# Optimization experiments

Hardware: AMD Instinct MI355X
Metric: run time of the kernel (lower is better)

The kernel has to match this reference:

```python
import jax, jax.numpy as jnp
import numpy as np

N_PDE = 4096
SENSOR_RANGE = 0.08
WINDOW = int(SENSOR_RANGE * N_PDE)   # 327
HALF = WINDOW // 2                   # 163
RESIZE_LEN = 20
FREQS = jnp.array([1.0, 2.0, 4.0, 8.0], dtype=jnp.float32)
EPS = 1e-6  # flax GroupNorm default epsilon
U_MAX, V_MAX = 40.0, 1.0
N_AGENTS = 262144


def setup_inputs() -> dict:
    key = jax.random.key(0)
    ks = jax.random.split(key, 16)

    def w(k, shape):
        fan_in = shape[0]
        return (jax.random.normal(k, shape, jnp.float32) / np.float32(np.sqrt(fan_in)))

    return {
        "z_curr": jax.random.normal(ks[0], (N_PDE,), jnp.float32),
        "z_target": jax.random.normal(ks[1], (N_PDE,), jnp.float32),
        "xi_curr": jax.random.uniform(ks[2], (N_AGENTS,), jnp.float32),
        # branch net (features=[256,256]), each layer: Dense + GroupNorm(1 group) + tanh
        "bW0": w(ks[3], (2 * RESIZE_LEN, 256)), "bb0": jnp.zeros((256,), jnp.float32),
        "bs0": jnp.ones((256,), jnp.float32), "bB0": jnp.zeros((256,), jnp.float32),
        "bW1": w(ks[4], (256, 256)), "bb1": jnp.zeros((256,), jnp.float32),
        "bs1": jnp.ones((256,), jnp.float32), "bB1": jnp.zeros((256,), jnp.float32),
        # trunk net: 8 -> 32 -> 32
        "tW0": w(ks[5], (8, 32)), "tb0": jnp.zeros((32,), jnp.float32),
        "tW1": w(ks[6], (32, 32)), "tb1": jnp.zeros((32,), jnp.float32),
        # combined head: (256+32) -> 32, then two 32 -> 1 heads
        "cW": w(ks[7], (256 + 32, 32)), "cb": jnp.zeros((32,), jnp.float32),
        "uW": w(ks[8], (32, 1)), "ub": jnp.zeros((1,), jnp.float32),
        "vW": w(ks[9], (32, 1)), "vb": jnp.zeros((1,), jnp.float32),
    }


def _local_obs(padded_error, xi):
    # per-agent dynamic slice + finite-difference gradient + bilinear resize
    center = (xi * (N_PDE - 1)).astype(jnp.int32) + HALF
    start = center - HALF
    p_err = jax.lax.dynamic_slice(padded_error, (start,), (WINDOW,))
    p_grad = jnp.gradient(p_err)
    p_err = jax.image.resize(p_err, (RESIZE_LEN,), method='bilinear')
    p_grad = jax.image.resize(p_grad, (RESIZE_LEN,), method='bilinear')
    return jnp.concatenate([p_err, p_grad])  # [40]


def _groupnorm1(x, scale, bias):
    # GroupNorm(num_groups=1) applied per-sample over the feature axis
    mu = jnp.mean(x, axis=-1, keepdims=True)
    var = jnp.var(x, axis=-1, keepdims=True)
    return (x - mu) * jax.lax.rsqrt(var + EPS) * scale + bias


def reference(z_curr, z_target, xi_curr,
              bW0, bb0, bs0, bB0, bW1, bb1, bs1, bB1,
              tW0, tb0, tW1, tb1, cW, cb, uW, ub, vW, vb):
    error = z_curr - z_target
    padded = jnp.pad(error, (HALF, HALF), mode='edge')  # [N_PDE + 2*HALF]

    patches = jax.vmap(lambda xi: _local_obs(padded, xi))(xi_curr)  # [A, 40]

    # branch net
    h = jnp.tanh(_groupnorm1(patches @ bW0 + bb0, bs0, bB0))  # [A, 256]
    h = jnp.tanh(_groupnorm1(h @ bW1 + bb1, bs1, bB1))        # [A, 256]

    # trunk net
    angle = xi_curr[:, None] * FREQS * jnp.pi                 # [A, 4]
    enc = jnp.concatenate([jnp.sin(angle), jnp.cos(angle)], axis=-1)  # [A, 8]
    enc = jnp.tanh(enc @ tW0 + tb0)
    enc = jnp.tanh(enc @ tW1 + tb1)                           # [A, 32]

    combined = jnp.concatenate([h, enc], axis=-1)             # [A, 288]
    x = jnp.tanh(combined @ cW + cb)                          # [A, 32]
    u_raw = (x @ uW + ub).squeeze(-1)
    v_raw = (x @ vW + vb).squeeze(-1)
    return (U_MAX * jnp.tanh(u_raw), V_MAX * jnp.tanh(v_raw))
```

## Files before the change

kernel.cpp:

```cpp
#include <hip/hip_runtime.h>

#define NP      4096
#define WINDOW  327
#define HALF    163
#define RL      20
#define NA      262144
#define GN_EPS  1e-6f
#define R       8
#define NBLK    (NP / R)
#define NT      512

__device__ __forceinline__ float tanh_fast(float x) {
  float e = __expf(2.0f * x);
  return 1.0f - 2.0f / (e + 1.0f);
}

__device__ __forceinline__ void wave_sum2(float& a, float& b) {
#pragma unroll
  for (int m = 1; m < 64; m <<= 1) {
    a += __shfl_xor(a, m, 64);
    b += __shfl_xor(b, m, 64);
  }
}

#define L_ESP   0
#define L_OBS   336
#define L_PART  0
#define L_HBUF  16384
#define L_HCL   18464
#define L_TOT   18752

__global__ __launch_bounds__(NT, 4) void dc_table(
    const float* __restrict__ zc,  const float* __restrict__ zt,
    const float* __restrict__ bW0, const float* __restrict__ bb0,
    const float* __restrict__ bs0, const float* __restrict__ bB0,
    const float* __restrict__ bW1, const float* __restrict__ bb1,
    const float* __restrict__ bs1, const float* __restrict__ bB1,
    const float* __restrict__ tW0, const float* __restrict__ tb0,
    const float* __restrict__ tW1, const float* __restrict__ tb1,
    const float* __restrict__ cW,  const float* __restrict__ cb,
    const float* __restrict__ uW,  const float* __restrict__ ub,
    const float* __restrict__ vW,  const float* __restrict__ vb,
    float* __restrict__ tbl)
{
  __shared__ __align__(16) float sm[L_TOT];
  float* espan = sm + L_ESP;
  float* obsT  = sm + L_OBS;
  float* part  = sm + L_PART;
  float* hbuf  = sm + L_HBUF;
  float* hcL   = sm + L_HCL;

  const int tid = threadIdx.x;
  const int w   = tid >> 6;
  const int l   = tid & 63;
  const int s0  = blockIdx.x * R;

  if (tid < WINDOW + R - 1) {
    int c = s0 - HALF + tid;
    c = c < 0 ? 0 : (c > NP - 1 ? NP - 1 : c);
    espan[tid] = zc[c] - zt[c];
  }
  __syncthreads();

  {
    const float INV  = (float)WINDOW / (float)RL;
    const float RINV = (float)RL / (float)WINDOW;
    const int sub = tid & 7;
    const int g8  = tid >> 3;
#pragma unroll
    for (int it = 0; it < 5; ++it) {
      int task = it * 64 + g8;
      int q = task % (2 * RL);
      int r = task / (2 * RL);
      int qq = (q < RL) ? q : q - RL;
      float xs = ((float)qq + 0.5f) * INV - 0.5f;
      int jlo = (int)ceilf(xs - INV);  if (jlo < 0) jlo = 0;
      int jhi = (int)floorf(xs + INV); if (jhi > WINDOW - 1) jhi = WINDOW - 1;
      const float* p = espan + r;
      float wsum = 0.0f, vsum = 0.0f;
      for (int j = jlo + sub; j <= jhi; j += 8) {
        float wq = 1.0f - fabsf(xs - (float)j) * RINV;
        float v;
        if (q < RL) {
          v = p[j];
        } else {
          v = (j == 0) ? (p[1] - p[0]) :
              (j == WINDOW - 1) ? (p[WINDOW - 1] - p[WINDOW - 2]) :
              0.5f * (p[j + 1] - p[j - 1]);
        }
        wsum += wq;
        vsum += wq * v;
      }
#pragma unroll
      for (int m = 1; m < 8; m <<= 1) {
        wsum += __shfl_xor(wsum, m, 64);
        vsum += __shfl_xor(vsum, m, 64);
      }
      if (sub == 0) obsT[q * 8 + r] = vsum / wsum;
    }
  }
  __syncthreads();

  float acc[R][4];

#pragma unroll
  for (int r = 0; r < R; ++r) { acc[r][0]=0.f; acc[r][1]=0.f; acc[r][2]=0.f; acc[r][3]=0.f; }
  for (int kk = 0; kk < 5; ++kk) {
    int k = w * 5 + kk;
    float4 wt = *(const float4*)&bW0[k * 256 + 4 * l];
    float4 o0 = *(const float4*)&obsT[k * 8];
    float4 o1 = *(const float4*)&obsT[k * 8 + 4];
    const float wv[4] = {wt.x, wt.y, wt.z, wt.w};
    const float ov[8] = {o0.x, o0.y, o0.z, o0.w, o1.x, o1.y, o1.z, o1.w};
#pragma unroll
    for (int r = 0; r < R; ++r)
#pragma unroll
      for (int j = 0; j < 4; ++j) acc[r][j] = fmaf(ov[r], wv[j], acc[r][j]);
  }
  __syncthreads();

#pragma unroll
  for (int r = 0; r < R; ++r)
    *(float4*)&part[w * 2048 + r * 256 + 4 * l] = make_float4(acc[r][0], acc[r][1], acc[r][2], acc[r][3]);
  __syncthreads();
  {
    float4 b0 = *(const float4*)&bb0[4 * l];
    float val[4] = {b0.x, b0.y, b0.z, b0.w};
#pragma unroll
    for (int w2 = 0; w2 < 8; ++w2) {
      float4 p0 = *(const float4*)&part[w2 * 2048 + w * 256 + 4 * l];
      val[0]+=p0.x; val[1]+=p0.y; val[2]+=p0.z; val[3]+=p0.w;
    }
    float s = 0.f, q = 0.f;
#pragma unroll
    for (int i = 0; i < 4; ++i) { s += val[i]; q += val[i] * val[i]; }
    wave_sum2(s, q);
    float mu  = s * (1.0f / 256.0f);
    float var = fmaxf(q * (1.0f / 256.0f) - mu * mu, 0.0f);
    float rv  = rsqrtf(var + GN_EPS);
    float4 sc0 = *(const float4*)&bs0[4 * l];
    float4 sh0 = *(const float4*)&bB0[4 * l];
    const float sc[4] = {sc0.x,sc0.y,sc0.z,sc0.w};
    const float sh[4] = {sh0.x,sh0.y,sh0.z,sh0.w};
    float h[4];
#pragma unroll
    for (int i = 0; i < 4; ++i) h[i] = tanh_fast((val[i] - mu) * rv * sc[i] + sh[i]);
    *(float4*)&hbuf[w * 260 + 4 * l] = make_float4(h[0], h[1], h[2], h[3]);
  }
  __syncthreads();

#pragma unroll
  for (int r = 0; r < R; ++r) { acc[r][0]=0.f; acc[r][1]=0.f; acc[r][2]=0.f; acc[r][3]=0.f; }
  for (int kk = 0; kk < 32; kk += 4) {
    int k0 = w * 32 + kk;
    float4 wt0 = *(const float4*)&bW1[(k0    ) * 256 + 4 * l];
    float4 wt1 = *(const float4*)&bW1[(k0 + 1) * 256 + 4 * l];
    float4 wt2 = *(const float4*)&bW1[(k0 + 2) * 256 + 4 * l];
    float4 wt3 = *(const float4*)&bW1[(k0 + 3) * 256 + 4 * l];
    float4 hr[R];
#pragma unroll
    for (int r = 0; r < R; ++r) hr[r] = *(const float4*)&hbuf[r * 260 + k0];
#pragma unroll
    for (int r = 0; r < R; ++r) {
      const float* hp = (const float*)&hr[r];
      acc[r][0] = fmaf(hp[0], wt0.x, acc[r][0]); acc[r][1] = fmaf(hp[0], wt0.y, acc[r][1]);
      acc[r][2] = fmaf(hp[0], wt0.z, acc[r][2]); acc[r][3] = fmaf(hp[0], wt0.w, acc[r][3]);
      acc[r][0] = fmaf(hp[1], wt1.x, acc[r][0]); acc[r][1] = fmaf(hp[1], wt1.y, acc[r][1]);
      acc[r][2] = fmaf(hp[1], wt1.z, acc[r][2]); acc[r][3] = fmaf(hp[1], wt1.w, acc[r][3]);
      acc[r][0] = fmaf(hp[2], wt2.x, acc[r][0]); acc[r][1] = fmaf(hp[2], wt2.y, acc[r][1]);
      acc[r][2] = fmaf(hp[2], wt2.z, acc[r][2]); acc[r][3] = fmaf(hp[2], wt2.w, acc[r][3]);
      acc[r][0] = fmaf(hp[3], wt3.x, acc[r][0]); acc[r][1] = fmaf(hp[3], wt3.y, acc[r][1]);
      acc[r][2] = fmaf(hp[3], wt3.z, acc[r][2]); acc[r][3] = fmaf(hp[3], wt3.w, acc[r][3]);
    }
  }

#pragma unroll
  for (int r = 0; r < R; ++r)
    *(float4*)&part[w * 2048 + r * 256 + 4 * l] = make_float4(acc[r][0], acc[r][1], acc[r][2], acc[r][3]);
  __syncthreads();
  {
    float4 b0 = *(const float4*)&bb1[4 * l];
    float val[4] = {b0.x, b0.y, b0.z, b0.w};
#pragma unroll
    for (int w2 = 0; w2 < 8; ++w2) {
      float4 p0 = *(const float4*)&part[w2 * 2048 + w * 256 + 4 * l];
      val[0]+=p0.x; val[1]+=p0.y; val[2]+=p0.z; val[3]+=p0.w;
    }
    float s = 0.f, q = 0.f;
#pragma unroll
    for (int i = 0; i < 4; ++i) { s += val[i]; q += val[i] * val[i]; }
    wave_sum2(s, q);
    float mu  = s * (1.0f / 256.0f);
    float var = fmaxf(q * (1.0f / 256.0f) - mu * mu, 0.0f);
    float rv  = rsqrtf(var + GN_EPS);
    float4 sc0 = *(const float4*)&bs1[4 * l];
    float4 sh0 = *(const float4*)&bB1[4 * l];
    const float sc[4] = {sc0.x,sc0.y,sc0.z,sc0.w};
    const float sh[4] = {sh0.x,sh0.y,sh0.z,sh0.w};
    float h[4];
#pragma unroll
    for (int i = 0; i < 4; ++i) h[i] = tanh_fast((val[i] - mu) * rv * sc[i] + sh[i]);
    *(float4*)&hbuf[w * 260 + 4 * l] = make_float4(h[0], h[1], h[2], h[3]);
  }
  __syncthreads();

  {
    int r  = w;
    int kg = l >> 3;
    int c  = (l & 7) * 4;
    float ga0 = 0.f, ga1 = 0.f, ga2 = 0.f, ga3 = 0.f;
#pragma unroll
    for (int ii = 0; ii < 8; ++ii) {
      int j  = (ii + kg) & 7;
      int kb = kg * 32 + 4 * j;
      float4 hv = *(const float4*)&hbuf[r * 260 + kb];
      const float hvv[4] = {hv.x, hv.y, hv.z, hv.w};
#pragma unroll
      for (int i2 = 0; i2 < 4; ++i2) {
        float4 cw = *(const float4*)&cW[(kb + i2) * 32 + c];
        ga0 = fmaf(hvv[i2], cw.x, ga0);
        ga1 = fmaf(hvv[i2], cw.y, ga1);
        ga2 = fmaf(hvv[i2], cw.z, ga2);
        ga3 = fmaf(hvv[i2], cw.w, ga3);
      }
    }
#pragma unroll
    for (int m = 8; m < 64; m <<= 1) {
      ga0 += __shfl_xor(ga0, m, 64);
      ga1 += __shfl_xor(ga1, m, 64);
      ga2 += __shfl_xor(ga2, m, 64);
      ga3 += __shfl_xor(ga3, m, 64);
    }
    if (l < 8) {
      float4 cbv = *(const float4*)&cb[c];
      *(float4*)&hcL[r * 36 + c] = make_float4(ga0 + cbv.x, ga1 + cbv.y, ga2 + cbv.z, ga3 + cbv.w);
    }
  }
  __syncthreads();

  if (tid < 128) {
    int v = tid >> 3, sub = tid & 7;
    int r = v >> 1, e = v & 1;
    int jg = s0 + r + e;
    float xe = (float)jg * (1.0f / 4095.0f);
    float enc[8];
#pragma unroll
    for (int k = 0; k < 4; ++k) {
      float fr = (float)(1 << k);
      float a = (xe * fr) * 3.14159265358979f;
      enc[k]     = sinf(a);
      enc[k + 4] = cosf(a);
    }
    int base = (tid & 63) & ~7;

    float t0v[4];
#pragma unroll
    for (int i = 0; i < 4; ++i) {
      int f = 4 * sub + i;
      float a = tb0[f];
#pragma unroll
      for (int k = 0; k < 8; ++k) a = fmaf(enc[k], tW0[k * 32 + f], a);
      t0v[i] = tanh_fast(a);
    }

    float t1v[4];
#pragma unroll
    for (int i = 0; i < 4; ++i) t1v[i] = tb1[4 * sub + i];
#pragma unroll
    for (int j8 = 0; j8 < 8; ++j8) {
#pragma unroll
      for (int i2 = 0; i2 < 4; ++i2) {
        float tv = __shfl(t0v[i2], base + j8, 64);
        int k = 4 * j8 + i2;
#pragma unroll
        for (int i = 0; i < 4; ++i) t1v[i] = fmaf(tv, tW1[k * 32 + 4 * sub + i], t1v[i]);
      }
    }
#pragma unroll
    for (int i = 0; i < 4; ++i) t1v[i] = tanh_fast(t1v[i]);

    float xvv[4];
#pragma unroll
    for (int i = 0; i < 4; ++i) xvv[i] = hcL[r * 36 + 4 * sub + i];
#pragma unroll
    for (int j8 = 0; j8 < 8; ++j8) {
#pragma unroll
      for (int i2 = 0; i2 < 4; ++i2) {
        float tv = __shfl(t1v[i2], base + j8, 64);
        int k = 4 * j8 + i2;
#pragma unroll
        for (int i = 0; i < 4; ++i) xvv[i] = fmaf(tv, cW[(256 + k) * 32 + 4 * sub + i], xvv[i]);
      }
    }
#pragma unroll
    for (int i = 0; i < 4; ++i) xvv[i] = tanh_fast(xvv[i]);

    float up = 0.f, vp = 0.f;
#pragma unroll
    for (int i = 0; i < 4; ++i) {
      up = fmaf(xvv[i], uW[4 * sub + i], up);
      vp = fmaf(xvv[i], vW[4 * sub + i], vp);
    }
#pragma unroll
    for (int m = 1; m < 8; m <<= 1) {
      up += __shfl_xor(up, m, 64);
      vp += __shfl_xor(vp, m, 64);
    }
    if (sub == 0) {
      int s = s0 + r;
      tbl[4 * s + e]     = 40.0f * tanh_fast(up + ub[0]);
      tbl[4 * s + 2 + e] = tanh_fast(vp + vb[0]);
    }
  }
}

__global__ __launch_bounds__(256) void dc_agents(
    const float* __restrict__ xi_curr, const float4* __restrict__ tbl,
    float* __restrict__ out)
{
  int a = blockIdx.x * 256 + threadIdx.x;
  float xi = xi_curr[a];
  float p = xi * 4095.0f;
  int s = (int)p;
  s = s > 4095 ? 4095 : s;
  float t = p - (float)s;
  float4 tb = tbl[s];
  out[a]      = fmaf(t, tb.y - tb.x, tb.x);
  out[NA + a] = fmaf(t, tb.w - tb.z, tb.z);
}

extern "C" void kernel_launch(void* const* d_in, const int* in_sizes, int n_in,
                              void* d_out, int out_size, void* d_ws, size_t ws_size,
                              hipStream_t stream) {
  const float* zc  = (const float*)d_in[0];
  const float* zt  = (const float*)d_in[1];
  const float* xi  = (const float*)d_in[2];
  const float* bW0 = (const float*)d_in[3];
  const float* bb0 = (const float*)d_in[4];
  const float* bs0 = (const float*)d_in[5];
  const float* bB0 = (const float*)d_in[6];
  const float* bW1 = (const float*)d_in[7];
  const float* bb1 = (const float*)d_in[8];
  const float* bs1 = (const float*)d_in[9];
  const float* bB1 = (const float*)d_in[10];
  const float* tW0 = (const float*)d_in[11];
  const float* tb0 = (const float*)d_in[12];
  const float* tW1 = (const float*)d_in[13];
  const float* tb1 = (const float*)d_in[14];
  const float* cW  = (const float*)d_in[15];
  const float* cb  = (const float*)d_in[16];
  const float* uW  = (const float*)d_in[17];
  const float* ub  = (const float*)d_in[18];
  const float* vW  = (const float*)d_in[19];
  const float* vb  = (const float*)d_in[20];

  float* tbl = (float*)d_ws;
  float* out = (float*)d_out;

  dc_table<<<NBLK, NT, 0, stream>>>(zc, zt, bW0, bb0, bs0, bB0,
                                    bW1, bb1, bs1, bB1,
                                    tW0, tb0, tW1, tb1, cW, cb,
                                    uW, ub, vW, vb, tbl);
  dc_agents<<<NA / 256, 256, 0, stream>>>(xi, (const float4*)tbl, out);
}
```

Before: 122.8 us.

## Stream bW1 into LDS with async double-buffered global_load_lds during layer-1 matmul

```diff
diff --git a/kernel.cpp b/kernel.cpp
--- a/kernel.cpp
+++ b/kernel.cpp
@@ -23,12 +23,23 @@
   }
 }
 
-#define L_ESP   0
-#define L_OBS   336
-#define L_PART  0
+__device__ __forceinline__ void stage16(const float* g, float* d) {
+  __builtin_amdgcn_global_load_lds(
+      (const __attribute__((address_space(1))) unsigned int*)g,
+      (__attribute__((address_space(3))) unsigned int*)d, 16, 0, 0);
+}
+
+#define WAITVM4() do { asm volatile("s_waitcnt vmcnt(4)" ::: "memory"); __builtin_amdgcn_sched_barrier(0); } while(0)
+#define WAITVM0() do { asm volatile("s_waitcnt vmcnt(0)" ::: "memory"); __builtin_amdgcn_sched_barrier(0); } while(0)
+#define SEAM_FENCE() do { asm volatile("" ::: "memory"); __builtin_amdgcn_sched_barrier(0); } while(0)
+
+#define L_WB    0
+#define L_PART  8192
 #define L_HBUF  16384
 #define L_HCL   18464
-#define L_TOT   18752
+#define L_ESP   18752
+#define L_OBS   19088
+#define L_TOT   19408
 
 __global__ __launch_bounds__(NT, 4) void dc_table(
     const float* __restrict__ zc,  const float* __restrict__ zt,
@@ -54,6 +65,15 @@
   const int w   = tid >> 6;
   const int l   = tid & 63;
   const int s0  = blockIdx.x * R;
+
+  auto issue_chunk = [&](int c) {
+    float* dst = sm + L_WB + ((c & 1) ? 8192 : 0) + (w << 10);
+    const float* src = bW1 + (((w << 5) + (c << 2)) << 8) + 4 * l;
+#pragma unroll
+    for (int j = 0; j < 4; ++j) stage16(src + (j << 8), dst + (j << 8));
+  };
+
+  issue_chunk(0);
 
   if (tid < WINDOW + R - 1) {
     int c = s0 - HALF + tid;
@@ -117,46 +137,52 @@
 #pragma unroll
       for (int j = 0; j < 4; ++j) acc[r][j] = fmaf(ov[r], wv[j], acc[r][j]);
   }
-  __syncthreads();
-
-#pragma unroll
-  for (int r = 0; r < R; ++r)
-    *(float4*)&part[w * 2048 + r * 256 + 4 * l] = make_float4(acc[r][0], acc[r][1], acc[r][2], acc[r][3]);
-  __syncthreads();
-  {
-    float4 b0 = *(const float4*)&bb0[4 * l];
-    float val[4] = {b0.x, b0.y, b0.z, b0.w};
-#pragma unroll
-    for (int w2 = 0; w2 < 8; ++w2) {
-      float4 p0 = *(const float4*)&part[w2 * 2048 + w * 256 + 4 * l];
-      val[0]+=p0.x; val[1]+=p0.y; val[2]+=p0.z; val[3]+=p0.w;
-    }
-    float s = 0.f, q = 0.f;
-#pragma unroll
-    for (int i = 0; i < 4; ++i) { s += val[i]; q += val[i] * val[i]; }
-    wave_sum2(s, q);
-    float mu  = s * (1.0f / 256.0f);
-    float var = fmaxf(q * (1.0f / 256.0f) - mu * mu, 0.0f);
-    float rv  = rsqrtf(var + GN_EPS);
-    float4 sc0 = *(const float4*)&bs0[4 * l];
-    float4 sh0 = *(const float4*)&bB0[4 * l];
-    const float sc[4] = {sc0.x,sc0.y,sc0.z,sc0.w};
-    const float sh[4] = {sh0.x,sh0.y,sh0.z,sh0.w};
-    float h[4];
-#pragma unroll
-    for (int i = 0; i < 4; ++i) h[i] = tanh_fast((val[i] - mu) * rv * sc[i] + sh[i]);
-    *(float4*)&hbuf[w * 260 + 4 * l] = make_float4(h[0], h[1], h[2], h[3]);
-  }
-  __syncthreads();
+
+#pragma unroll
+  for (int p = 0; p < 2; ++p) {
+#pragma unroll
+    for (int r4 = 0; r4 < 4; ++r4)
+      *(float4*)&part[(w << 10) + (r4 << 8) + 4 * l] =
+        make_float4(acc[4*p+r4][0], acc[4*p+r4][1], acc[4*p+r4][2], acc[4*p+r4][3]);
+    __syncthreads();
+    if (w < 4) {
+      int row = 4 * p + w;
+      float4 b0 = *(const float4*)&bb0[4 * l];
+      float val[4] = {b0.x, b0.y, b0.z, b0.w};
+#pragma unroll
+      for (int w2 = 0; w2 < 8; ++w2) {
+        float4 p0 = *(const float4*)&part[(w2 << 10) + (w << 8) + 4 * l];
+        val[0]+=p0.x; val[1]+=p0.y; val[2]+=p0.z; val[3]+=p0.w;
+      }
+      float s = 0.f, q = 0.f;
+#pragma unroll
+      for (int i = 0; i < 4; ++i) { s += val[i]; q += val[i] * val[i]; }
+      wave_sum2(s, q);
+      float mu  = s * (1.0f / 256.0f);
+      float var = fmaxf(q * (1.0f / 256.0f) - mu * mu, 0.0f);
+      float rv  = rsqrtf(var + GN_EPS);
+      float4 sc0 = *(const float4*)&bs0[4 * l];
+      float4 sh0 = *(const float4*)&bB0[4 * l];
+      const float sc[4] = {sc0.x,sc0.y,sc0.z,sc0.w};
+      const float sh[4] = {sh0.x,sh0.y,sh0.z,sh0.w};
+      float h[4];
+#pragma unroll
+      for (int i = 0; i < 4; ++i) h[i] = tanh_fast((val[i] - mu) * rv * sc[i] + sh[i]);
+      *(float4*)&hbuf[row * 260 + 4 * l] = make_float4(h[0], h[1], h[2], h[3]);
+    }
+    __syncthreads();
+  }
 
 #pragma unroll
   for (int r = 0; r < R; ++r) { acc[r][0]=0.f; acc[r][1]=0.f; acc[r][2]=0.f; acc[r][3]=0.f; }
-  for (int kk = 0; kk < 32; kk += 4) {
-    int k0 = w * 32 + kk;
-    float4 wt0 = *(const float4*)&bW1[(k0    ) * 256 + 4 * l];
-    float4 wt1 = *(const float4*)&bW1[(k0 + 1) * 256 + 4 * l];
-    float4 wt2 = *(const float4*)&bW1[(k0 + 2) * 256 + 4 * l];
-    float4 wt3 = *(const float4*)&bW1[(k0 + 3) * 256 + 4 * l];
+
+  auto compute_chunk = [&](int c) {
+    const float* wb = sm + L_WB + ((c & 1) ? 8192 : 0) + (w << 10);
+    const int k0 = (w << 5) + (c << 2);
+    float4 wt0 = *(const float4*)&wb[      4 * l];
+    float4 wt1 = *(const float4*)&wb[256 + 4 * l];
+    float4 wt2 = *(const float4*)&wb[512 + 4 * l];
+    float4 wt3 = *(const float4*)&wb[768 + 4 * l];
     float4 hr[R];
 #pragma unroll
     for (int r = 0; r < R; ++r) hr[r] = *(const float4*)&hbuf[r * 260 + k0];
@@ -172,37 +198,52 @@
       acc[r][0] = fmaf(hp[3], wt3.x, acc[r][0]); acc[r][1] = fmaf(hp[3], wt3.y, acc[r][1]);
       acc[r][2] = fmaf(hp[3], wt3.z, acc[r][2]); acc[r][3] = fmaf(hp[3], wt3.w, acc[r][3]);
     }
-  }
-
-#pragma unroll
-  for (int r = 0; r < R; ++r)
-    *(float4*)&part[w * 2048 + r * 256 + 4 * l] = make_float4(acc[r][0], acc[r][1], acc[r][2], acc[r][3]);
-  __syncthreads();
-  {
-    float4 b0 = *(const float4*)&bb1[4 * l];
-    float val[4] = {b0.x, b0.y, b0.z, b0.w};
-#pragma unroll
-    for (int w2 = 0; w2 < 8; ++w2) {
-      float4 p0 = *(const float4*)&part[w2 * 2048 + w * 256 + 4 * l];
-      val[0]+=p0.x; val[1]+=p0.y; val[2]+=p0.z; val[3]+=p0.w;
-    }
-    float s = 0.f, q = 0.f;
-#pragma unroll
-    for (int i = 0; i < 4; ++i) { s += val[i]; q += val[i] * val[i]; }
-    wave_sum2(s, q);
-    float mu  = s * (1.0f / 256.0f);
-    float var = fmaxf(q * (1.0f / 256.0f) - mu * mu, 0.0f);
-    float rv  = rsqrtf(var + GN_EPS);
-    float4 sc0 = *(const float4*)&bs1[4 * l];
-    float4 sh0 = *(const float4*)&bB1[4 * l];
-    const float sc[4] = {sc0.x,sc0.y,sc0.z,sc0.w};
-    const float sh[4] = {sh0.x,sh0.y,sh0.z,sh0.w};
-    float h[4];
-#pragma unroll
-    for (int i = 0; i < 4; ++i) h[i] = tanh_fast((val[i] - mu) * rv * sc[i] + sh[i]);
-    *(float4*)&hbuf[w * 260 + 4 * l] = make_float4(h[0], h[1], h[2], h[3]);
-  }
-  __syncthreads();
+  };
+
+  for (int c = 0; c < 7; ++c) {
+    SEAM_FENCE();
+    issue_chunk(c + 1);
+    WAITVM4();
+    compute_chunk(c);
+  }
+  SEAM_FENCE();
+  WAITVM0();
+  compute_chunk(7);
+
+#pragma unroll
+  for (int p = 0; p < 2; ++p) {
+#pragma unroll
+    for (int r4 = 0; r4 < 4; ++r4)
+      *(float4*)&part[(w << 10) + (r4 << 8) + 4 * l] =
+        make_float4(acc[4*p+r4][0], acc[4*p+r4][1], acc[4*p+r4][2], acc[4*p+r4][3]);
+    __syncthreads();
+    if (w < 4) {
+      int row = 4 * p + w;
+      float4 b0 = *(const float4*)&bb1[4 * l];
+      float val[4] = {b0.x, b0.y, b0.z, b0.w};
+#pragma unroll
+      for (int w2 = 0; w2 < 8; ++w2) {
+        float4 p0 = *(const float4*)&part[(w2 << 10) + (w << 8) + 4 * l];
+        val[0]+=p0.x; val[1]+=p0.y; val[2]+=p0.z; val[3]+=p0.w;
+      }
+      float s = 0.f, q = 0.f;
+#pragma unroll
+      for (int i = 0; i < 4; ++i) { s += val[i]; q += val[i] * val[i]; }
+      wave_sum2(s, q);
+      float mu  = s * (1.0f / 256.0f);
+      float var = fmaxf(q * (1.0f / 256.0f) - mu * mu, 0.0f);
+      float rv  = rsqrtf(var + GN_EPS);
+      float4 sc0 = *(const float4*)&bs1[4 * l];
+      float4 sh0 = *(const float4*)&bB1[4 * l];
+      const float sc[4] = {sc0.x,sc0.y,sc0.z,sc0.w};
+      const float sh[4] = {sh0.x,sh0.y,sh0.z,sh0.w};
+      float h[4];
+#pragma unroll
+      for (int i = 0; i < 4; ++i) h[i] = tanh_fast((val[i] - mu) * rv * sc[i] + sh[i]);
+      *(float4*)&hbuf[row * 260 + 4 * l] = make_float4(h[0], h[1], h[2], h[3]);
+    }
+    __syncthreads();
+  }
 
   {
     int r  = w;
```

After: 125.3 us. 1.02x slower.
